# Kernel tuning notes

Hardware: AMD Instinct MI355X
Metric: run time of the kernel (lower is better)

Reference implementation:

```python
import jax, jax.numpy as jnp
import numpy as np

NUM_GRAPHS = 512

def setup_inputs() -> dict:
    key = jax.random.key(0)
    ks = jax.random.split(key, 6)
    N, E, D = 100000, 1600000, 128
    x = jax.random.normal(ks[0], (N, D), dtype=jnp.float32)
    edge_index = jax.random.randint(ks[1], (2, E), 0, N, dtype=jnp.int64)
    batch = jnp.sort(jax.random.randint(ks[2], (N,), 0, NUM_GRAPHS, dtype=jnp.int64))
    scale = 1.0 / np.sqrt(D)
    Ws = jax.random.normal(ks[3], (4, D, D), dtype=jnp.float32) * scale
    bs = jnp.zeros((4, D), dtype=jnp.float32)
    Wl = jax.random.normal(ks[4], (D, 1), dtype=jnp.float32) * scale
    bl = jnp.zeros((1,), dtype=jnp.float32)
    return {"x": x, "edge_index": edge_index, "batch": batch,
            "Ws": Ws, "bs": bs, "Wl": Wl, "bl": bl}

def reference(x, edge_index, batch, Ws, bs, Wl, bl):
    N = x.shape[0]
    loops = jnp.arange(N, dtype=edge_index.dtype)
    # GCNConv: add self-loops, symmetric normalization D^{-1/2} A D^{-1/2}
    row = jnp.concatenate([edge_index[0], loops])  # source nodes
    col = jnp.concatenate([edge_index[1], loops])  # target nodes
    deg = jax.ops.segment_sum(jnp.ones_like(col, dtype=x.dtype), col, num_segments=N)
    dinv = jnp.where(deg > 0, jax.lax.rsqrt(jnp.maximum(deg, 1.0)), 0.0)
    norm = dinv[row] * dinv[col]  # [E+N]
    h = x
    for i in range(Ws.shape[0]):
        h = h @ Ws[i]                                   # [N, D]
        msg = h[row] * norm[:, None]                    # gather + scale, [E+N, D]
        h = jax.ops.segment_sum(msg, col, num_segments=N) + bs[i]
        h = jax.nn.relu(h)                              # dropout is identity in eval
    # global_mean_pool over graphs
    sums = jax.ops.segment_sum(h, batch, num_segments=NUM_GRAPHS)
    cnt = jax.ops.segment_sum(jnp.ones((N,), h.dtype), batch, num_segments=NUM_GRAPHS)
    pooled = sums / jnp.maximum(cnt, 1.0)[:, None]      # [G, D]
    return pooled @ Wl + bl                             # [G, 1]
```

## Files before the change

kernel.cpp:

```cpp
#include <hip/hip_runtime.h>


constexpr int D = 128;
constexpr int NGRAPH = 512;
constexpr int CHUNK = 4096;
constexpr int BSH = 9;
constexpr int OP = 136;

typedef __attribute__((ext_vector_type(8))) short bf16x8;
typedef __attribute__((ext_vector_type(4))) float f32x4;
typedef int i32x4u __attribute__((ext_vector_type(4), aligned(4)));

__device__ __forceinline__ float bf2f(unsigned short b) {
    return __uint_as_float(((unsigned int)b) << 16);
}
__device__ __forceinline__ unsigned short f2bf(float f) {
    unsigned int u = __float_as_uint(f);
    u += 0x7FFFu + ((u >> 16) & 1u);
    return (unsigned short)(u >> 16);
}

__global__ __launch_bounds__(256) void setup_all(
        const float4* __restrict__ x4, ushort4* __restrict__ hb, int n4, int CB,
        const float* __restrict__ W, unsigned short* __restrict__ Wt,
        const int* __restrict__ ec, int E, int* __restrict__ bucketCnt) {
    __shared__ int h[256];
    const int t = threadIdx.x;
    const int b = blockIdx.x;
    if (b < CB) {
        int i = b * 256 + t;
        if (i < n4) {
            float4 v = x4[i];
            ushort4 o;
            o.x = f2bf(v.x); o.y = f2bf(v.y); o.z = f2bf(v.z); o.w = f2bf(v.w);
            hb[i] = o;
        }
    } else if (b < CB + 256) {
        int idx = (b - CB) * 256 + t;
        int i = idx >> 14;
        int rem = idx & 16383;
        int k = rem >> 7, c = rem & 127;
        Wt[(i << 14) + c * 128 + k] = f2bf(W[idx]);
    } else {
        h[t] = 0;
        __syncthreads();
        const int e0 = (b - CB - 256) * CHUNK;
        const int cnt = min(CHUNK, E - e0);
        for (int i = t; i < cnt; i += 256) atomicAdd(&h[ec[e0 + i] >> BSH], 1);
        __syncthreads();
        if (h[t]) atomicAdd(&bucketCnt[t], h[t]);
    }
}

__global__ __launch_bounds__(256) void bucket_scan(const int* __restrict__ bucketCnt,
                                                   int* __restrict__ bucketBase,
                                                   int* __restrict__ globCursor) {
    __shared__ int s[256];
    const int t = threadIdx.x;
    int v = bucketCnt[t];
    s[t] = v; __syncthreads();
    for (int off = 1; off < 256; off <<= 1) {
        int x = (t >= off) ? s[t - off] : 0;
        __syncthreads();
        s[t] += x;
        __syncthreads();
    }
    int excl = s[t] - v;
    bucketBase[t] = excl;
    globCursor[t] = excl;
}

__global__ __launch_bounds__(256) void scatter_pairs(const int* __restrict__ er,
                                                     const int* __restrict__ ec, int E,
                                                     int* __restrict__ globCursor,
                                                     int2* __restrict__ pairs) {
    __shared__ int h[256], lbase[256], cur[256], segd[256], s[256];
    __shared__ int2 stage[CHUNK];
    const int t = threadIdx.x;
    const int e0 = blockIdx.x * CHUNK;
    const int cnt = min(CHUNK, E - e0);

    h[t] = 0;
    __syncthreads();
    for (int i = t; i < cnt; i += 256) atomicAdd(&h[ec[e0 + i] >> BSH], 1);
    __syncthreads();
    int v = h[t];
    s[t] = v; __syncthreads();
    for (int off = 1; off < 256; off <<= 1) {
        int x = (t >= off) ? s[t - off] : 0;
        __syncthreads();
        s[t] += x;
        __syncthreads();
    }
    lbase[t] = s[t] - v;
    cur[t] = s[t] - v;
    segd[t] = atomicAdd(&globCursor[t], v) - lbase[t];
    __syncthreads();
    for (int i = t; i < cnt; i += 256) {
        int c = ec[e0 + i];
        int b = c >> BSH;
        int p = atomicAdd(&cur[b], 1);
        stage[p] = make_int2(er[e0 + i], c);
    }
    __syncthreads();
    for (int i = t; i < cnt; i += 256) {
        int2 pr = stage[i];
        int b = pr.y >> BSH;
        pairs[segd[b] + i] = pr;
    }
}

__global__ __launch_bounds__(256) void fill_csr(const int2* __restrict__ pairs,
                                                const int* __restrict__ bucketBase,
                                                const int* __restrict__ bucketCnt,
                                                int N, int E, int NBUCK,
                                                int* __restrict__ rowptr,
                                                float* __restrict__ dinv,
                                                int* __restrict__ srcs,
                                                unsigned short* __restrict__ Hb0) {
    __shared__ int hist[512], lofs[512], s[256];
    const int t = threadIdx.x;
    const int b = blockIdx.x;
    const int c0 = b << BSH;
    const int base = bucketBase[b];
    const int cnt = bucketCnt[b];
    const int2* pp = pairs + base;

    hist[t] = 0; hist[t + 256] = 0;
    __syncthreads();
    for (int i = t; i < cnt; i += 256) atomicAdd(&hist[pp[i].y - c0], 1);
    __syncthreads();
    int a0 = hist[2 * t], a1 = hist[2 * t + 1];
    s[t] = a0 + a1; __syncthreads();
    for (int off = 1; off < 256; off <<= 1) {
        int x = (t >= off) ? s[t - off] : 0;
        __syncthreads();
        s[t] += x;
        __syncthreads();
    }
    int excl = s[t] - (a0 + a1);
    lofs[2 * t] = excl;
    lofs[2 * t + 1] = excl + a0;
    __syncthreads();
    const int nn = min(512, N - c0);
    for (int i = t; i < nn; i += 256) {
        rowptr[c0 + i] = base + lofs[i];
        dinv[c0 + i] = rsqrtf((float)hist[i] + 1.0f);
    }
    if (b == NBUCK - 1 && t == 0) rowptr[N] = E;
    __syncthreads();
    for (int i = t; i < cnt; i += 256) {
        int2 pr = pp[i];
        int p = atomicAdd(&lofs[pr.y - c0], 1);
        srcs[base + p] = pr.x;
    }
    unsigned int* Hrow = (unsigned int*)Hb0 + (size_t)c0 * 64;
    for (int i = t; i < nn * 64; i += 256) {
        int r = i >> 6;
        float dv = rsqrtf((float)hist[r] + 1.0f);
        unsigned int v = Hrow[i];
        unsigned short lo = f2bf(bf2f((unsigned short)(v & 0xFFFFu)) * dv);
        unsigned short hi = f2bf(bf2f((unsigned short)(v >> 16)) * dv);
        Hrow[i] = ((unsigned int)hi << 16) | lo;
    }
}

__global__ __launch_bounds__(64, 4) void layer_fused(
        const int* __restrict__ rowptr, const int* __restrict__ srcs,
        const float* __restrict__ dinv, const unsigned short* __restrict__ H,
        const unsigned short* __restrict__ Wt, const float* __restrict__ bias,
        unsigned short* __restrict__ Hn, float* __restrict__ dots,
        const float* __restrict__ Wl, int N, int writeDots) {
    __shared__ __align__(16) unsigned short U[16 * OP];
    const int lane = threadIdx.x;
    const int row16 = lane & 15;
    const int quad = lane >> 4;
    const int r0 = blockIdx.x * 16;
    const bf16x8* H8 = (const bf16x8*)H;
    const int gl = row16;

#pragma unroll 1
    for (int sstep = 0; sstep < 4; ++sstep) {
        const int rt = quad * 4 + sstep;
        const int row = r0 + rt;
        float acc[8] = {0.f, 0.f, 0.f, 0.f, 0.f, 0.f, 0.f, 0.f};
        float sn = 0.f;
        if (row < N) {
            sn = dinv[row];
            int j = rowptr[row];
            const int end = rowptr[row + 1];
            bf16x8 hv = H8[(size_t)row * 16 + gl];
#pragma unroll
            for (int k = 0; k < 8; ++k) acc[k] = bf2f((unsigned short)hv[k]);
            const int ne = end - j;
            const int nb = (ne + 7) >> 3;
            if (nb > 0) {
                i32x4u sA0, sA1, sB0, sB1;
                {
                    const i32x4u* sp = (const i32x4u*)(srcs + j);
                    sA0 = sp[0]; sA1 = sp[1];
                }
                if (nb > 1) {
                    const i32x4u* sp = (const i32x4u*)(srcs + j + 8);
                    sB0 = sp[0]; sB1 = sp[1];
                }
                bf16x8 hc[8], hn[8];
#pragma unroll
                for (int t = 0; t < 8; ++t) {
                    int idx = (t < 4) ? sA0[t] : sA1[t - 4];
                    int rr = (t < ne) ? idx : row;
                    hc[t] = H8[(size_t)rr * 16 + gl];
                }
#pragma unroll 1
                for (int b = 0; b < nb; ++b) {
                    if (b + 1 < nb) {
                        const int remn = ne - (b + 1) * 8;
                        int rn[8];
#pragma unroll
                        for (int t = 0; t < 8; ++t) {
                            int idx = (t < 4) ? sB0[t] : sB1[t - 4];
                            rn[t] = (t < remn) ? idx : row;
                        }
                        if (b + 2 < nb) {
                            const i32x4u* sp = (const i32x4u*)(srcs + j + (b + 2) * 8);
                            sB0 = sp[0]; sB1 = sp[1];
                        }
#pragma unroll
                        for (int t = 0; t < 8; ++t)
                            hn[t] = H8[(size_t)rn[t] * 16 + gl];
                    }
                    const int rem = ne - b * 8;
#pragma unroll
                    for (int t = 0; t < 8; ++t) {
                        const float w = (t < rem) ? 1.f : 0.f;
#pragma unroll
                        for (int k = 0; k < 8; ++k)
                            acc[k] = fmaf(w, bf2f((unsigned short)hc[t][k]), acc[k]);
                    }
#pragma unroll
                    for (int t = 0; t < 8; ++t) hc[t] = hn[t];
                }
            }
        }
        bf16x8 o;
#pragma unroll
        for (int k = 0; k < 8; ++k) o[k] = (short)f2bf(sn * acc[k]);
        *(bf16x8*)(U + rt * 128 + ((gl ^ rt) << 3)) = o;
    }
    __syncthreads();

    bf16x8 a0[4];
#pragma unroll
    for (int kc = 0; kc < 4; ++kc) {
        const int ph = (kc * 4 + quad) ^ row16;
        a0[kc] = *(const bf16x8*)(U + row16 * 128 + ph * 8);
    }
    __syncthreads();

    float dv[4];
    if (!writeDots) {
#pragma unroll
        for (int i = 0; i < 4; ++i) {
            int ra = r0 + quad * 4 + i;
            dv[i] = (ra < N) ? dinv[ra] : 0.f;
        }
    }

    float rd[4] = {0.f, 0.f, 0.f, 0.f};
#pragma unroll
    for (int ct = 0; ct < 8; ++ct) {
        const int col = ct * 16 + row16;
        const bf16x8* wc = (const bf16x8*)(Wt + (size_t)col * 128);
        f32x4 acc0 = {0.f, 0.f, 0.f, 0.f};
#pragma unroll
        for (int kc = 0; kc < 4; ++kc) {
            const bf16x8 wf = wc[kc * 4 + quad];
            acc0 = __builtin_amdgcn_mfma_f32_16x16x32_bf16(a0[kc], wf, acc0, 0, 0, 0);
        }
        const float bv = bias[col];
        if (writeDots) {
            const float wl = Wl[col];
#pragma unroll
            for (int i = 0; i < 4; ++i) rd[i] += fmaxf(acc0[i] + bv, 0.f) * wl;
        } else {
#pragma unroll
            for (int i = 0; i < 4; ++i)
                U[(quad * 4 + i) * OP + col] = f2bf(dv[i] * fmaxf(acc0[i] + bv, 0.f));
        }
    }

    if (writeDots) {
#pragma unroll
        for (int m = 1; m < 16; m <<= 1)
#pragma unroll
            for (int i = 0; i < 4; ++i) rd[i] += __shfl_xor(rd[i], m, 64);
        if (row16 == 0) {
#pragma unroll
            for (int i = 0; i < 4; ++i) dots[r0 + quad * 4 + i] = rd[i];
        }
    } else {
        __syncthreads();
#pragma unroll
        for (int i = 0; i < 4; ++i) {
            int idx = i * 64 + lane;
            int row = idx >> 4, c8 = idx & 15;
            bf16x8 v = *(const bf16x8*)(U + row * OP + c8 * 8);
            *(bf16x8*)(Hn + (size_t)(r0 + row) * 128 + c8 * 8) = v;
        }
    }
}

__global__ __launch_bounds__(256) void pool_graphs(const float* __restrict__ dots,
                                                   const int* __restrict__ batch, int N,
                                                   const float* __restrict__ bl,
                                                   float* __restrict__ out) {
    __shared__ int bounds[2];
    __shared__ float red[4];
    const int g = blockIdx.x;
    const int t = threadIdx.x;
    if (t < 2) {
        int key = g + t;
        int lo = 0, hi = N;
        while (lo < hi) {
            int mid = (lo + hi) >> 1;
            if (batch[mid] < key) lo = mid + 1; else hi = mid;
        }
        bounds[t] = lo;
    }
    __syncthreads();
    const int lo = bounds[0], hi = bounds[1];
    float s = 0.f;
    for (int i = lo + t; i < hi; i += 256) s += dots[i];
#pragma unroll
    for (int off = 32; off > 0; off >>= 1) s += __shfl_down(s, off, 64);
    if ((t & 63) == 0) red[t >> 6] = s;
    __syncthreads();
    if (t == 0) {
        float tot = red[0] + red[1] + red[2] + red[3];
        int cnt = hi - lo;
        out[g] = tot / (float)(cnt > 0 ? cnt : 1) + bl[0];
    }
}

extern "C" void kernel_launch(void* const* d_in, const int* in_sizes, int n_in,
                              void* d_out, int out_size, void* d_ws, size_t ws_size,
                              hipStream_t stream) {
    const float* x     = (const float*)d_in[0];
    const int*   eidx  = (const int*)d_in[1];
    const int*   batch = (const int*)d_in[2];
    const float* Ws    = (const float*)d_in[3];
    const float* bs    = (const float*)d_in[4];
    const float* Wl    = (const float*)d_in[5];
    const float* bl    = (const float*)d_in[6];
    (void)n_in; (void)out_size;

    const int N = in_sizes[0] / D;
    const int E = in_sizes[1] / 2;
    const int* er = eidx;
    const int* ec = eidx + E;
    const int NBUCK = (N + 511) >> BSH;
    const int NCHUNK = (E + CHUNK - 1) / CHUNK;

    const int Npad = (N + 127) & ~127;
    const size_t hBytes = (size_t)Npad * D * sizeof(unsigned short);
    auto al = [](size_t v) { return (v + 255) & ~(size_t)255; };
    char* base = (char*)d_ws;
    size_t off = 0;

    unsigned short* Hb0 = (unsigned short*)base; off = al(hBytes);
    int* bucketCnt  = (int*)(base + off);
    int* globCursor = bucketCnt + 256;
    off = al(off + 512 * sizeof(int));
    int*   bucketBase = (int*)(base + off);  off = al(off + 256 * sizeof(int));
    float* dinv   = (float*)(base + off);    off = al(off + (size_t)Npad * sizeof(float));
    float* dots   = (float*)(base + off);    off = al(off + (size_t)Npad * sizeof(float));
    int*   rowptr = (int*)(base + off);      off = al(off + (size_t)(Npad + 64) * sizeof(int));
    int*   srcs   = (int*)(base + off);      off = al(off + (size_t)E * sizeof(int) + 64);
    unsigned short* Wt = (unsigned short*)(base + off);   off = al(off + 4 * 128 * 128 * sizeof(unsigned short));

    const bool twoBuf = ws_size >= off + hBytes;
    unsigned short* Hb1 = twoBuf ? (unsigned short*)(base + off)
                                 : (unsigned short*)d_in[0];
    int2* pairs = (int2*)Hb1;
    unsigned short* hb[2] = { Hb0, Hb1 };

    hipMemsetAsync(bucketCnt, 0, 256 * sizeof(int), stream);
    const int n4 = N * D / 4;
    const int CB = (n4 + 255) / 256;
    setup_all<<<CB + 256 + NCHUNK, 256, 0, stream>>>((const float4*)x, (ushort4*)Hb0,
                                                     n4, CB, Ws, Wt, ec, E, bucketCnt);

    bucket_scan<<<1, 256, 0, stream>>>(bucketCnt, bucketBase, globCursor);
    scatter_pairs<<<NCHUNK, 256, 0, stream>>>(er, ec, E, globCursor, pairs);
    fill_csr<<<NBUCK, 256, 0, stream>>>(pairs, bucketBase, bucketCnt, N, E, NBUCK,
                                        rowptr, dinv, srcs, Hb0);

    for (int i = 0; i < 4; ++i) {
        const unsigned short* Hc = hb[i & 1];
        unsigned short* Hn = hb[(i + 1) & 1];
        layer_fused<<<Npad / 16, 64, 0, stream>>>(rowptr, srcs, dinv, Hc,
                                                  Wt + (size_t)i * D * D,
                                                  bs + (size_t)i * D, Hn, dots, Wl,
                                                  N, (i == 3) ? 1 : 0);
    }

    pool_graphs<<<NGRAPH, 256, 0, stream>>>(dots, batch, N, bl, (float*)d_out);
}
```

Baseline: 512.9 us.

## Pack four independent waves per layer block and split x scaling into its own kernel

The fused layer kernel now runs four independent 16-row waves per 256-thread block, each with its own shared-memory tile, and drops the block barriers because each wave only touches its own tile. This cuts the block count fourfold and is meant to improve scheduling and occupancy of the gather-plus-MFMA layer kernel. Scaling the initial bf16 features by dinv moves out of fill_csr into a separate vectorized elementwise kernel, which costs an extra launch but uses 16-byte accesses and removes the tail loop from the bucket kernel. Npad must be a multiple of 64, or guards must cover the extra rows, for the new grid to stay correct.

After: 486.0 us. 5.2% less time.

```diff
diff --git a/kernel.cpp b/kernel.cpp
--- a/kernel.cpp
+++ b/kernel.cpp
@@ -116,8 +116,7 @@
                                                 int N, int E, int NBUCK,
                                                 int* __restrict__ rowptr,
                                                 float* __restrict__ dinv,
-                                                int* __restrict__ srcs,
-                                                unsigned short* __restrict__ Hb0) {
+                                                int* __restrict__ srcs) {
     __shared__ int hist[512], lofs[512], s[256];
     const int t = threadIdx.x;
     const int b = blockIdx.x;
@@ -154,28 +153,39 @@
         int p = atomicAdd(&lofs[pr.y - c0], 1);
         srcs[base + p] = pr.x;
     }
-    unsigned int* Hrow = (unsigned int*)Hb0 + (size_t)c0 * 64;
-    for (int i = t; i < nn * 64; i += 256) {
-        int r = i >> 6;
-        float dv = rsqrtf((float)hist[r] + 1.0f);
-        unsigned int v = Hrow[i];
-        unsigned short lo = f2bf(bf2f((unsigned short)(v & 0xFFFFu)) * dv);
-        unsigned short hi = f2bf(bf2f((unsigned short)(v >> 16)) * dv);
-        Hrow[i] = ((unsigned int)hi << 16) | lo;
-    }
-}
-
-__global__ __launch_bounds__(64, 4) void layer_fused(
+}
+
+__global__ __launch_bounds__(256) void scale_x(uint4* __restrict__ Hb0,
+                                               const float* __restrict__ dinv,
+                                               int nq) {
+    int i = blockIdx.x * 256 + threadIdx.x;
+    if (i >= nq) return;
+    float dv = dinv[i >> 4];
+    uint4 v = Hb0[i];
+    unsigned int* p = (unsigned int*)&v;
+#pragma unroll
+    for (int k = 0; k < 4; ++k) {
+        unsigned int d = p[k];
+        unsigned short lo = f2bf(bf2f((unsigned short)(d & 0xFFFFu)) * dv);
+        unsigned short hi = f2bf(bf2f((unsigned short)(d >> 16)) * dv);
+        p[k] = ((unsigned int)hi << 16) | lo;
+    }
+    Hb0[i] = v;
+}
+
+__global__ __launch_bounds__(256, 4) void layer_fused(
         const int* __restrict__ rowptr, const int* __restrict__ srcs,
         const float* __restrict__ dinv, const unsigned short* __restrict__ H,
         const unsigned short* __restrict__ Wt, const float* __restrict__ bias,
         unsigned short* __restrict__ Hn, float* __restrict__ dots,
         const float* __restrict__ Wl, int N, int writeDots) {
-    __shared__ __align__(16) unsigned short U[16 * OP];
-    const int lane = threadIdx.x;
+    __shared__ __align__(16) unsigned short u[4][16 * OP];
+    const int wave = threadIdx.x >> 6;
+    const int lane = threadIdx.x & 63;
     const int row16 = lane & 15;
     const int quad = lane >> 4;
-    const int r0 = blockIdx.x * 16;
+    const int r0 = blockIdx.x * 64 + wave * 16;
+    unsigned short* U = u[wave];
     const bf16x8* H8 = (const bf16x8*)H;
     const int gl = row16;
 
@@ -247,7 +257,6 @@
         for (int k = 0; k < 8; ++k) o[k] = (short)f2bf(sn * acc[k]);
         *(bf16x8*)(U + rt * 128 + ((gl ^ rt) << 3)) = o;
     }
-    __syncthreads();
 
     bf16x8 a0[4];
 #pragma unroll
@@ -255,7 +264,6 @@
         const int ph = (kc * 4 + quad) ^ row16;
         a0[kc] = *(const bf16x8*)(U + row16 * 128 + ph * 8);
     }
-    __syncthreads();
 
     float dv[4];
     if (!writeDots) {
@@ -299,7 +307,6 @@
             for (int i = 0; i < 4; ++i) dots[r0 + quad * 4 + i] = rd[i];
         }
     } else {
-        __syncthreads();
 #pragma unroll
         for (int i = 0; i < 4; ++i) {
             int idx = i * 64 + lane;
@@ -393,15 +400,17 @@
     bucket_scan<<<1, 256, 0, stream>>>(bucketCnt, bucketBase, globCursor);
     scatter_pairs<<<NCHUNK, 256, 0, stream>>>(er, ec, E, globCursor, pairs);
     fill_csr<<<NBUCK, 256, 0, stream>>>(pairs, bucketBase, bucketCnt, N, E, NBUCK,
-                                        rowptr, dinv, srcs, Hb0);
+                                        rowptr, dinv, srcs);
+    const int nq = N * 16;
+    scale_x<<<(nq + 255) / 256, 256, 0, stream>>>((uint4*)Hb0, dinv, nq);
 
     for (int i = 0; i < 4; ++i) {
         const unsigned short* Hc = hb[i & 1];
         unsigned short* Hn = hb[(i + 1) & 1];
-        layer_fused<<<Npad / 16, 64, 0, stream>>>(rowptr, srcs, dinv, Hc,
-                                                  Wt + (size_t)i * D * D,
-                                                  bs + (size_t)i * D, Hn, dots, Wl,
-                                                  N, (i == 3) ? 1 : 0);
+        layer_fused<<<Npad / 64, 256, 0, stream>>>(rowptr, srcs, dinv, Hc,
+                                                   Wt + (size_t)i * D * D,
+                                                   bs + (size_t)i * D, Hn, dots, Wl,
+                                                   N, (i == 3) ? 1 : 0);
     }
 
     pool_graphs<<<NGRAPH, 256, 0, stream>>>(dots, batch, N, bl, (float*)d_out);
```
